# Kernel tuning notes

Hardware: AMD Instinct MI355X
Metric: run time of the kernel (lower is better)

Reference implementation:

```python
import jax, jax.numpy as jnp
from jax import lax
import numpy as np

GROUPS = 32

def setup_inputs() -> dict:
    key = jax.random.key(0)
    ks = jax.random.split(key, 12)
    B, C, H, O, N = 4, 256, 256, 256, 4096
    s = 0.02  # small init scale to keep logits in a stable range
    x  = jax.random.normal(ks[0], (B, C, N), dtype=jnp.float32)
    Wk = jax.random.normal(ks[1], (H, C), dtype=jnp.float32) * s
    bk = jax.random.normal(ks[2], (H,), dtype=jnp.float32) * s
    Wq = jax.random.normal(ks[3], (H, C), dtype=jnp.float32) * s
    bq = jax.random.normal(ks[4], (H,), dtype=jnp.float32) * s
    W1 = jax.random.normal(ks[5], (H, C), dtype=jnp.float32) * s
    b1 = jax.random.normal(ks[6], (H,), dtype=jnp.float32) * s
    # grouped conv1d kernel: (out_ch, in_ch // groups, kw) in 'OIH' layout
    W2 = jax.random.normal(ks[7], (H, H // GROUPS, 3), dtype=jnp.float32) * s
    b2 = jax.random.normal(ks[8], (H,), dtype=jnp.float32) * s
    W3 = jax.random.normal(ks[9], (O, H), dtype=jnp.float32) * s
    b3 = jax.random.normal(ks[10], (O,), dtype=jnp.float32) * s
    return {"x": x, "Wk": Wk, "bk": bk, "Wq": Wq, "bq": bq,
            "W1": W1, "b1": b1, "W2": W2, "b2": b2, "W3": W3, "b3": b3}


def reference(x, Wk, bk, Wq, bq, W1, b1, W2, b2, W3, b3):
    # k: 1x1 conv then permute(0,2,1) -> [B, N, H]
    k = jnp.einsum('hc,bcn->bnh', Wk, x) + bk
    # q: 1x1 conv -> [B, H, N]
    q = jnp.einsum('hc,bcn->bhn', Wq, x) + bq[None, :, None]
    # sim = softmax(k @ q, dim=-2): softmax over the FIRST N axis (rows)
    sim = jax.nn.softmax(jnp.einsum('bnh,bhm->bnm', k, q), axis=-2)  # [B, N, N]
    # v path: 1x1 conv -> grouped 3-tap conv (pad=1) -> ReLU -> 1x1 conv
    v1 = jnp.einsum('hc,bcn->bhn', W1, x) + b1[None, :, None]
    v2 = lax.conv_general_dilated(
        v1, W2, window_strides=(1,), padding='SAME',
        feature_group_count=GROUPS,
        dimension_numbers=('NCH', 'OIH', 'NCH')) + b2[None, :, None]
    v2 = jax.nn.relu(v2)
    v = jnp.einsum('oh,bhn->bon', W3, v2) + b3[None, :, None]  # [B, O, N]
    # out = v @ sim -> [B, O, N]
    return jnp.einsum('bon,bnm->bom', v, sim)
```

## Files before the change

### kernel.cpp

```cpp
#include <hip/hip_runtime.h>


#define B_ 4
#define C_ 256
#define H_ 256
#define O_ 256
#define N_ 4096
#define NSPLIT 4
#define SPAN (N_ / NSPLIT)
#define ITERS (SPAN / 32)

typedef short short8 __attribute__((ext_vector_type(8)));
typedef float floatx4 __attribute__((ext_vector_type(4)));
typedef float floatx16 __attribute__((ext_vector_type(16)));
typedef unsigned uint2v __attribute__((ext_vector_type(2)));

__device__ __forceinline__ unsigned short f2bf(float f) {
  unsigned u = __float_as_uint(f);
  u = (u + 0x7fffu + ((u >> 16) & 1u)) >> 16;
  return (unsigned short)u;
}
__device__ __forceinline__ float bf2f(unsigned short u) {
  return __uint_as_float(((unsigned)u) << 16);
}
__device__ __forceinline__ floatx4 mfma16(short8 a, short8 b, floatx4 c) {
  return __builtin_amdgcn_mfma_f32_16x16x32_bf16(a, b, c, 0, 0, 0);
}
__device__ __forceinline__ floatx16 mfma32(short8 a, short8 b, floatx16 c) {
  return __builtin_amdgcn_mfma_f32_32x32x16_bf16(a, b, c, 0, 0, 0);
}
__device__ __forceinline__ unsigned pack2bf(float a, float b) {
  return __builtin_amdgcn_perm(__float_as_uint(b) + 0x8000u,
                               __float_as_uint(a) + 0x8000u, 0x07060302u);
}

__global__ __launch_bounds__(256) void prep_w_kernel(
    const float* __restrict__ Wk, const float* __restrict__ Wq,
    const float* __restrict__ W1, const float* __restrict__ W3,
    unsigned short* __restrict__ wk, unsigned short* __restrict__ wq,
    unsigned short* __restrict__ w1, unsigned short* __restrict__ w3) {
  const int i = blockIdx.x * 256 + threadIdx.x;
  wk[i] = f2bf(Wk[i]);
  wq[i] = f2bf(Wq[i]);
  w1[i] = f2bf(W1[i]);
  w3[i] = f2bf(W3[i]);
}

__global__ __launch_bounds__(256) void gemm1_kernel(
    const float* __restrict__ x,
    const unsigned short* __restrict__ wk,
    const float* __restrict__ bk, const float* __restrict__ bq,
    const float* __restrict__ b1,
    unsigned short* __restrict__ ko, unsigned short* __restrict__ qo,
    unsigned short* __restrict__ v1o) {
  __shared__ unsigned short xL[32][264];

  const int blk  = blockIdx.x;
  const int b    = blk >> 7;
  const int nc   = blk & 127;
  const int n032 = nc * 32;
  const int t    = threadIdx.x;

  {
    const int c0 = t >> 3;
    const int nq = t & 7;
    const float* xb = x + ((size_t)b * C_) * N_ + n032 + nq * 4;
#pragma unroll
    for (int i = 0; i < 8; ++i) {
      const int c = c0 + i * 32;
      const floatx4 v = *reinterpret_cast<const floatx4*>(xb + (size_t)c * N_);
#pragma unroll
      for (int j = 0; j < 4; ++j) xL[nq * 4 + j][c] = f2bf(v[j]);
    }
  }
  __syncthreads();

  const int ln  = t & 63;
  const int wv  = t >> 6;
  const int m32 = ln & 31;
  const int hl  = ln >> 5;

  int   uoff[6];
  float ubias[6];
  int   uop[6], utt[6];
#pragma unroll
  for (int u = 0; u < 6; ++u) {
    const int gu = wv * 6 + u;
    const int op = gu >> 3;
    const int tt = gu & 7;
    uop[u] = op;
    utt[u] = tt;
    uoff[u] = op * 65536 + (tt * 32 + m32) * 256 + hl * 8;
    const float* bp = (op == 0) ? bk : ((op == 1) ? bq : b1);
    ubias[u] = bp[tt * 32 + m32];
  }

  floatx16 acc[6];
#pragma unroll
  for (int u = 0; u < 6; ++u)
#pragma unroll
    for (int r = 0; r < 16; ++r) acc[u][r] = 0.f;

#pragma unroll
  for (int ks = 0; ks < 16; ++ks) {
    short8 af = *reinterpret_cast<const short8*>(&xL[m32][ks * 16 + hl * 8]);
#pragma unroll
    for (int u = 0; u < 6; ++u) {
      short8 bf = *reinterpret_cast<const short8*>(wk + uoff[u] + ks * 16);
      acc[u] = mfma32(af, bf, acc[u]);
    }
  }

#pragma unroll
  for (int u = 0; u < 6; ++u) {
    const int h = utt[u] * 32 + m32;
    if (uop[u] == 0) {
      unsigned short* kb = ko + ((size_t)(b * 128 + nc)) * 8192;
      const int eh = (h >> 4) * 512 + ((h >> 3) & 1) * 256 + (h & 7);
#pragma unroll
      for (int r = 0; r < 16; ++r) {
        const int nl = (r & 3) + 8 * (r >> 2) + 4 * hl;
        kb[eh + nl * 8] = f2bf(acc[u][r] + ubias[u]);
      }
    } else {
      unsigned short* o = (uop[u] == 1) ? qo : v1o;
#pragma unroll
      for (int r = 0; r < 16; ++r) {
        const int n = n032 + (r & 3) + 8 * (r >> 2) + 4 * hl;
        o[((size_t)(b * N_ + n)) * H_ + h] = f2bf(acc[u][r] + ubias[u]);
      }
    }
  }
}

__global__ __launch_bounds__(256) void convgemm2_kernel(
    const unsigned short* __restrict__ v1, const float* __restrict__ W2,
    const float* __restrict__ b2, const unsigned short* __restrict__ w3,
    const float* __restrict__ b3, unsigned short* __restrict__ vo) {
  __shared__ unsigned short v2L[32][264];

  const int h   = threadIdx.x;
  const int blk = blockIdx.x;
  const int b   = blk >> 7;
  const int nc  = blk & 127;
  const int n0  = nc * 32;
  const int g8  = h & ~7;

  {
    float w[24];
#pragma unroll
    for (int i = 0; i < 24; ++i) w[i] = W2[h * 24 + i];
    const float bias = b2[h];
    const unsigned short* vb = v1 + (size_t)b * (N_ * H_) + g8;

    float fp[8], fc[8], fn[8];
    if (n0 == 0) {
#pragma unroll
      for (int i = 0; i < 8; ++i) fp[i] = 0.f;
    } else {
      short8 u = *reinterpret_cast<const short8*>(vb + (size_t)(n0 - 1) * H_);
#pragma unroll
      for (int i = 0; i < 8; ++i) fp[i] = bf2f((unsigned short)u[i]);
    }
    {
      short8 u = *reinterpret_cast<const short8*>(vb + (size_t)n0 * H_);
#pragma unroll
      for (int i = 0; i < 8; ++i) fc[i] = bf2f((unsigned short)u[i]);
    }
#pragma unroll 1
    for (int ns = 0; ns < 32; ++ns) {
      const int n = n0 + ns;
      if (n + 1 < N_) {
        short8 u = *reinterpret_cast<const short8*>(vb + (size_t)(n + 1) * H_);
#pragma unroll
        for (int i = 0; i < 8; ++i) fn[i] = bf2f((unsigned short)u[i]);
      } else {
#pragma unroll
        for (int i = 0; i < 8; ++i) fn[i] = 0.f;
      }
      float a = bias;
#pragma unroll
      for (int i = 0; i < 8; ++i)
        a += w[i * 3] * fp[i] + w[i * 3 + 1] * fc[i] + w[i * 3 + 2] * fn[i];
      v2L[ns][h] = f2bf(fmaxf(a, 0.f));
#pragma unroll
      for (int i = 0; i < 8; ++i) { fp[i] = fc[i]; fc[i] = fn[i]; }
    }
  }
  __syncthreads();

  const int ln = threadIdx.x & 63;
  const int wv = threadIdx.x >> 6;
  const int m  = ln & 31;
  const int hl = ln >> 5;

  floatx16 acc2[2];
#pragma unroll
  for (int ot = 0; ot < 2; ++ot)
#pragma unroll
    for (int r = 0; r < 16; ++r) acc2[ot][r] = 0.f;

#pragma unroll
  for (int ks = 0; ks < 16; ++ks) {
    short8 bfr = *reinterpret_cast<const short8*>(&v2L[m][ks * 16 + hl * 8]);
#pragma unroll
    for (int ot = 0; ot < 2; ++ot) {
      const int o0 = wv * 64 + ot * 32;
      short8 afr = *reinterpret_cast<const short8*>(
          w3 + (o0 + m) * H_ + ks * 16 + hl * 8);
      acc2[ot] = mfma32(afr, bfr, acc2[ot]);
    }
  }

  const int kn = (m >> 4) & 1;
  const int nl = m & 15;
  unsigned short* vkn = vo + ((size_t)(b * 128 + nc) * 2 + kn) * 4096;
#pragma unroll
  for (int ot = 0; ot < 2; ++ot)
#pragma unroll
    for (int r = 0; r < 16; ++r) {
      const int o = wv * 64 + ot * 32 + (r & 3) + 8 * (r >> 2) + 4 * hl;
      vkn[(o >> 5) * 512 + (nl >> 3) * 256 + (o & 31) * 8 + (nl & 7)] =
          f2bf(acc2[ot][r] + b3[o]);
    }
}

__global__ __launch_bounds__(512, 2) void attn_kernel(
    const unsigned short* __restrict__ kbf, const unsigned short* __restrict__ qbf,
    const unsigned short* __restrict__ vbf,
    unsigned short* __restrict__ pacc, float* __restrict__ pml) {
  __shared__ __attribute__((aligned(16))) char smem[7][16384];

  const int tid = threadIdx.x;
  const int ln  = tid & 63;
  const int wv  = tid >> 6;
  const int gid = blockIdx.x;
  const int b   = gid & 3;
  const int s   = (gid >> 2) & 3;
  const int mt256 = gid >> 4;
  const int mt32  = mt256 * 8 + wv;
  const int m0  = mt32 * 32;
  const int m   = ln & 31;
  const int hl  = ln >> 5;
  const bool grpB = (wv >= 4);
  const int lane_base = ln * 16;

  const unsigned short* qrow = qbf + ((size_t)b * N_ + m0 + m) * H_ + hl * 8;
  short8 qf[16];
#pragma unroll
  for (int ks = 0; ks < 16; ++ks)
    qf[ks] = *reinterpret_cast<const short8*>(qrow + ks * 16);

  floatx16 acc[8];
#pragma unroll
  for (int t = 0; t < 8; ++t)
#pragma unroll
    for (int r = 0; r < 16; ++r) acc[t][r] = 0.f;
  float Lp = 0.f;

  const size_t row0 = (size_t)(b * 128 + s * 32);

  auto stage = [&](int nc) {
    const char* kg = (const char*)(kbf + (row0 + nc) * 8192);
    const char* vg = (const char*)(vbf + (row0 + nc) * 8192);
    char* lk = &smem[nc % 3][0];
    char* lv = &smem[3 + (nc & 3)][0];
#pragma unroll
    for (int j = 0; j < 2; ++j) {
      const int ofs = j * 8192 + tid * 16;
      __builtin_amdgcn_global_load_lds(
          (const __attribute__((address_space(1))) void*)(kg + ofs),
          (__attribute__((address_space(3))) void*)(lk + ofs), 16, 0, 0);
      __builtin_amdgcn_global_load_lds(
          (const __attribute__((address_space(1))) void*)(vg + ofs),
          (__attribute__((address_space(3))) void*)(lv + ofs), 16, 0, 0);
    }
  };

  short8 pf0, pf1;

  auto qk = [&](const char* sk) -> floatx16 {
    floatx16 sacc;
#pragma unroll
    for (int r = 0; r < 16; ++r) sacc[r] = 0.f;
    __builtin_amdgcn_s_setprio(1);
#pragma unroll
    for (int ks = 0; ks < 16; ++ks) {
      short8 kf = *reinterpret_cast<const short8*>(sk + lane_base + ks * 1024);
      sacc = mfma32(kf, qf[ks], sacc);
    }
    __builtin_amdgcn_s_setprio(0);
    return sacc;
  };
  auto pv = [&](const char* sv) {
    __builtin_amdgcn_s_setprio(1);
#pragma unroll
    for (int ot = 0; ot < 8; ++ot) {
      short8 vf0 = *reinterpret_cast<const short8*>(sv + lane_base + ot * 1024);
      short8 vf1 = *reinterpret_cast<const short8*>(
          sv + lane_base + 8192 + ot * 1024);
      acc[ot] = mfma32(vf0, pf0, acc[ot]);
      acc[ot] = mfma32(vf1, pf1, acc[ot]);
    }
    __builtin_amdgcn_s_setprio(0);
  };
  auto softmax = [&](floatx16 sacc) {
#if __has_builtin(__builtin_amdgcn_permlane32_swap)
    unsigned d[8];
#pragma unroll
    for (int i = 0; i < 8; ++i) {
      const float a = __expf(sacc[2 * i]);
      const float bb = __expf(sacc[2 * i + 1]);
      Lp += a + bb;
      d[i] = pack2bf(a, bb);
    }
#pragma unroll
    for (int g = 0; g < 2; ++g) {
      uint2v r0 = __builtin_amdgcn_permlane32_swap(d[4 * g + 0], d[4 * g + 2],
                                                   false, false);
      uint2v r1 = __builtin_amdgcn_permlane32_swap(d[4 * g + 1], d[4 * g + 3],
                                                   false, false);
      d[4 * g + 0] = r0.x; d[4 * g + 2] = r0.y;
      d[4 * g + 1] = r1.x; d[4 * g + 3] = r1.y;
    }
    union { unsigned u[4]; short8 s8; } c0, c1;
    c0.u[0] = d[0]; c0.u[1] = d[1]; c0.u[2] = d[2]; c0.u[3] = d[3];
    c1.u[0] = d[4]; c1.u[1] = d[5]; c1.u[2] = d[6]; c1.u[3] = d[7];
    pf0 = c0.s8;
    pf1 = c1.s8;
#else
    float pv_[16];
#pragma unroll
    for (int r = 0; r < 16; ++r) { pv_[r] = __expf(sacc[r]); Lp += pv_[r]; }
    unsigned wpk[8];
#pragma unroll
    for (int r4 = 0; r4 < 4; ++r4) {
      wpk[r4]     = pack2bf(pv_[r4], pv_[r4 + 4]);
      wpk[r4 + 4] = pack2bf(pv_[r4 + 8], pv_[r4 + 12]);
    }
    const int hlsh = hl * 16;
#pragma unroll
    for (int j = 0; j < 8; ++j) {
      const int srcLane = m + ((j >> 2) << 5);
      const int u0 = __shfl((int)wpk[j & 3],       srcLane);
      const int u1 = __shfl((int)wpk[(j & 3) + 4], srcLane);
      pf0[j] = (short)((unsigned)u0 >> hlsh);
      pf1[j] = (short)((unsigned)u1 >> hlsh);
    }
#endif
  };

  stage(0);
  stage(1);

#pragma unroll 1
  for (int nc = 0; nc < ITERS; ++nc) {
    if (nc + 1 < ITERS) {
      asm volatile("s_waitcnt vmcnt(4)\n\ts_barrier" ::: "memory");
    } else {
      asm volatile("s_waitcnt vmcnt(0)\n\ts_barrier" ::: "memory");
    }
    __builtin_amdgcn_sched_barrier(0);
    if (nc + 2 < ITERS) stage(nc + 2);

    const char* sk = &smem[nc % 3][0];

    if (!grpB) {
      floatx16 sacc = qk(sk);
      softmax(sacc);
      pv(&smem[3 + (nc & 3)][0]);
    } else {
      if (nc > 0) pv(&smem[3 + ((nc - 1) & 3)][0]);
      floatx16 sacc = qk(sk);
      softmax(sacc);
    }
  }
  if (grpB) pv(&smem[3 + ((ITERS - 1) & 3)][0]);

  float Lv = Lp + __shfl_xor(Lp, 32);
  const float invL = 1.f / Lv;

  const int pwid = (b * 128 + mt32) * NSPLIT + s;
  unsigned short* pa = pacc + (size_t)pwid * (O_ * 32);
#pragma unroll
  for (int ot = 0; ot < 8; ++ot)
#pragma unroll
    for (int r = 0; r < 16; ++r) {
      const int o = ot * 32 + (r & 3) + 8 * (r >> 2) + 4 * hl;
      pa[o * 32 + m] = f2bf(acc[ot][r] * invL);
    }
  if (hl == 0) pml[pwid * 32 + m] = Lv;
}

__global__ __launch_bounds__(256) void combine_kernel(
    const unsigned short* __restrict__ pacc, const float* __restrict__ pml,
    float* __restrict__ out) {
  const int blk = blockIdx.x;
  const int b   = blk >> 7;
  const int mw  = blk & 127;
  const int o   = threadIdx.x;
  const int base = (b * 128 + mw) * NSPLIT;

  __shared__ float w[NSPLIT][32];
  if (threadIdx.x < 32) {
    const int c = threadIdx.x;
    float L[NSPLIT], sum = 0.f;
#pragma unroll
    for (int sp = 0; sp < NSPLIT; ++sp) {
      L[sp] = pml[(base + sp) * 32 + c];
      sum += L[sp];
    }
    const float inv = 1.f / sum;
#pragma unroll
    for (int sp = 0; sp < NSPLIT; ++sp) w[sp][c] = L[sp] * inv;
  }
  __syncthreads();

  float res[32];
#pragma unroll
  for (int c = 0; c < 32; ++c) res[c] = 0.f;
#pragma unroll
  for (int sp = 0; sp < NSPLIT; ++sp) {
    const unsigned short* pa =
        pacc + (size_t)(base + sp) * (O_ * 32) + o * 32;
#pragma unroll
    for (int c8 = 0; c8 < 4; ++c8) {
      short8 u = *reinterpret_cast<const short8*>(pa + c8 * 8);
#pragma unroll
      for (int i = 0; i < 8; ++i)
        res[c8 * 8 + i] =
            fmaf(w[sp][c8 * 8 + i], bf2f((unsigned short)u[i]), res[c8 * 8 + i]);
    }
  }
  float* ob = out + ((size_t)(b * O_ + o)) * N_ + mw * 32;
#pragma unroll
  for (int c4 = 0; c4 < 8; ++c4) {
    floatx4 v4 = {res[c4 * 4], res[c4 * 4 + 1], res[c4 * 4 + 2], res[c4 * 4 + 3]};
    *reinterpret_cast<floatx4*>(ob + c4 * 4) = v4;
  }
}

extern "C" void kernel_launch(void* const* d_in, const int* in_sizes, int n_in,
                              void* d_out, int out_size, void* d_ws, size_t ws_size,
                              hipStream_t stream) {
  const float* x  = (const float*)d_in[0];
  const float* Wk = (const float*)d_in[1];
  const float* bk = (const float*)d_in[2];
  const float* Wq = (const float*)d_in[3];
  const float* bq = (const float*)d_in[4];
  const float* W1 = (const float*)d_in[5];
  const float* b1 = (const float*)d_in[6];
  const float* W2 = (const float*)d_in[7];
  const float* b2 = (const float*)d_in[8];
  const float* W3 = (const float*)d_in[9];
  const float* b3 = (const float*)d_in[10];
  float* out = (float*)d_out;

  char* ws = (char*)d_ws;
  const size_t SZ = (size_t)B_ * N_ * H_ * sizeof(unsigned short);
  unsigned short* wkbf = (unsigned short*)(ws);
  unsigned short* wqbf = (unsigned short*)(ws + 131072);
  unsigned short* w1bf = (unsigned short*)(ws + 262144);
  unsigned short* w3bf = (unsigned short*)(ws + 393216);
  char* base = ws + 524288;
  unsigned short* kbf  = (unsigned short*)(base);
  unsigned short* qbf  = (unsigned short*)(base + SZ);
  unsigned short* vbf  = (unsigned short*)(base + 2 * SZ);
  unsigned short* v1bf = (unsigned short*)(base + 3 * SZ);
  unsigned short* pacc = (unsigned short*)(base + 3 * SZ);
  float*          pml  = (float*)(base + 7 * SZ);

  prep_w_kernel<<<256, 256, 0, stream>>>(
      Wk, Wq, W1, W3, wkbf, wqbf, w1bf, w3bf);
  gemm1_kernel<<<512, 256, 0, stream>>>(x, wkbf, bk, bq, b1,
                                        kbf, qbf, v1bf);
  convgemm2_kernel<<<512, 256, 0, stream>>>(v1bf, W2, b2, w3bf, b3, vbf);
  attn_kernel<<<256, 512, 0, stream>>>(kbf, qbf, vbf, pacc, pml);
  combine_kernel<<<512, 256, 0, stream>>>(pacc, pml, out);
}
```

Measured before the change: 221.2 us.

## Fuse projection GEMM, grouped conv and W3 GEMM into one kernel with halo

```diff
diff --git a/kernel.cpp b/kernel.cpp
--- a/kernel.cpp
+++ b/kernel.cpp
@@ -22,9 +22,6 @@
 }
 __device__ __forceinline__ float bf2f(unsigned short u) {
   return __uint_as_float(((unsigned)u) << 16);
-}
-__device__ __forceinline__ floatx4 mfma16(short8 a, short8 b, floatx4 c) {
-  return __builtin_amdgcn_mfma_f32_16x16x32_bf16(a, b, c, 0, 0, 0);
 }
 __device__ __forceinline__ floatx16 mfma32(short8 a, short8 b, floatx16 c) {
   return __builtin_amdgcn_mfma_f32_32x32x16_bf16(a, b, c, 0, 0, 0);
@@ -46,14 +43,18 @@
   w3[i] = f2bf(W3[i]);
 }
 
-__global__ __launch_bounds__(256) void gemm1_kernel(
+__global__ __launch_bounds__(256) void fused1_kernel(
     const float* __restrict__ x,
     const unsigned short* __restrict__ wk,
     const float* __restrict__ bk, const float* __restrict__ bq,
     const float* __restrict__ b1,
+    const float* __restrict__ W2, const float* __restrict__ b2,
+    const unsigned short* __restrict__ w3, const float* __restrict__ b3,
     unsigned short* __restrict__ ko, unsigned short* __restrict__ qo,
-    unsigned short* __restrict__ v1o) {
-  __shared__ unsigned short xL[32][264];
+    unsigned short* __restrict__ vo) {
+  __shared__ unsigned short xL[34][264];
+  __shared__ unsigned short v1L[34][264];
+  __shared__ unsigned short v2L[32][264];
 
   const int blk  = blockIdx.x;
   const int b    = blk >> 7;
@@ -70,8 +71,17 @@
       const int c = c0 + i * 32;
       const floatx4 v = *reinterpret_cast<const floatx4*>(xb + (size_t)c * N_);
 #pragma unroll
-      for (int j = 0; j < 4; ++j) xL[nq * 4 + j][c] = f2bf(v[j]);
-    }
+      for (int j = 0; j < 4; ++j) xL[1 + nq * 4 + j][c] = f2bf(v[j]);
+    }
+  }
+  {
+    const int c = t;
+    const float lv =
+        (n032 == 0) ? 0.f : x[((size_t)(b * C_ + c)) * N_ + n032 - 1];
+    const float rv =
+        (n032 + 32 >= N_) ? 0.f : x[((size_t)(b * C_ + c)) * N_ + n032 + 32];
+    xL[0][c] = f2bf(lv);
+    xL[33][c] = f2bf(rv);
   }
   __syncthreads();
 
@@ -80,104 +90,100 @@
   const int m32 = ln & 31;
   const int hl  = ln >> 5;
 
-  int   uoff[6];
-  float ubias[6];
-  int   uop[6], utt[6];
-#pragma unroll
-  for (int u = 0; u < 6; ++u) {
-    const int gu = wv * 6 + u;
-    const int op = gu >> 3;
-    const int tt = gu & 7;
-    uop[u] = op;
-    utt[u] = tt;
-    uoff[u] = op * 65536 + (tt * 32 + m32) * 256 + hl * 8;
+  {
+    const int op    = (wv <= 1) ? wv : 2;
+    const int abase = (wv <= 1) ? 1 : ((wv == 2) ? 0 : 2);
     const float* bp = (op == 0) ? bk : ((op == 1) ? bq : b1);
-    ubias[u] = bp[tt * 32 + m32];
-  }
-
-  floatx16 acc[6];
-#pragma unroll
-  for (int u = 0; u < 6; ++u)
-#pragma unroll
-    for (int r = 0; r < 16; ++r) acc[u][r] = 0.f;
-
-#pragma unroll
-  for (int ks = 0; ks < 16; ++ks) {
-    short8 af = *reinterpret_cast<const short8*>(&xL[m32][ks * 16 + hl * 8]);
-#pragma unroll
-    for (int u = 0; u < 6; ++u) {
-      short8 bf = *reinterpret_cast<const short8*>(wk + uoff[u] + ks * 16);
-      acc[u] = mfma32(af, bf, acc[u]);
-    }
-  }
-
-#pragma unroll
-  for (int u = 0; u < 6; ++u) {
-    const int h = utt[u] * 32 + m32;
-    if (uop[u] == 0) {
+
+    float ubias[8];
+    int   uoff[8];
+#pragma unroll
+    for (int u = 0; u < 8; ++u) {
+      uoff[u]  = op * 65536 + (u * 32 + m32) * 256 + hl * 8;
+      ubias[u] = bp[u * 32 + m32];
+    }
+
+    floatx16 acc[8];
+#pragma unroll
+    for (int u = 0; u < 8; ++u)
+#pragma unroll
+      for (int r = 0; r < 16; ++r) acc[u][r] = 0.f;
+
+#pragma unroll
+    for (int ks = 0; ks < 16; ++ks) {
+      short8 af =
+          *reinterpret_cast<const short8*>(&xL[abase + m32][ks * 16 + hl * 8]);
+#pragma unroll
+      for (int u = 0; u < 8; ++u) {
+        short8 bf = *reinterpret_cast<const short8*>(wk + uoff[u] + ks * 16);
+        acc[u] = mfma32(af, bf, acc[u]);
+      }
+    }
+
+    if (wv == 0) {
       unsigned short* kb = ko + ((size_t)(b * 128 + nc)) * 8192;
-      const int eh = (h >> 4) * 512 + ((h >> 3) & 1) * 256 + (h & 7);
-#pragma unroll
-      for (int r = 0; r < 16; ++r) {
-        const int nl = (r & 3) + 8 * (r >> 2) + 4 * hl;
-        kb[eh + nl * 8] = f2bf(acc[u][r] + ubias[u]);
+#pragma unroll
+      for (int u = 0; u < 8; ++u) {
+        const int h = u * 32 + m32;
+        const int eh = (h >> 4) * 512 + ((h >> 3) & 1) * 256 + (h & 7);
+#pragma unroll
+        for (int r = 0; r < 16; ++r) {
+          const int nl = (r & 3) + 8 * (r >> 2) + 4 * hl;
+          kb[eh + nl * 8] = f2bf(acc[u][r] + ubias[u]);
+        }
+      }
+    } else if (wv == 1) {
+#pragma unroll
+      for (int u = 0; u < 8; ++u) {
+        const int h = u * 32 + m32;
+#pragma unroll
+        for (int r = 0; r < 16; ++r) {
+          const int n = n032 + (r & 3) + 8 * (r >> 2) + 4 * hl;
+          qo[((size_t)(b * N_ + n)) * H_ + h] = f2bf(acc[u][r] + ubias[u]);
+        }
       }
     } else {
-      unsigned short* o = (uop[u] == 1) ? qo : v1o;
-#pragma unroll
-      for (int r = 0; r < 16; ++r) {
-        const int n = n032 + (r & 3) + 8 * (r >> 2) + 4 * hl;
-        o[((size_t)(b * N_ + n)) * H_ + h] = f2bf(acc[u][r] + ubias[u]);
-      }
-    }
-  }
-}
-
-__global__ __launch_bounds__(256) void convgemm2_kernel(
-    const unsigned short* __restrict__ v1, const float* __restrict__ W2,
-    const float* __restrict__ b2, const unsigned short* __restrict__ w3,
-    const float* __restrict__ b3, unsigned short* __restrict__ vo) {
-  __shared__ unsigned short v2L[32][264];
-
-  const int h   = threadIdx.x;
-  const int blk = blockIdx.x;
-  const int b   = blk >> 7;
-  const int nc  = blk & 127;
-  const int n0  = nc * 32;
-  const int g8  = h & ~7;
+      const int cofs = (wv == 2) ? 0 : 2;
+#pragma unroll
+      for (int u = 0; u < 8; ++u) {
+        const int h = u * 32 + m32;
+#pragma unroll
+        for (int r = 0; r < 16; ++r) {
+          const int col = cofs + (r & 3) + 8 * (r >> 2) + 4 * hl;
+          v1L[col][h] = f2bf(acc[u][r] + ubias[u]);
+        }
+      }
+    }
+  }
+  __syncthreads();
+
+  if (n032 == 0) v1L[0][t] = 0;
+  if (n032 + 32 >= N_) v1L[33][t] = 0;
+  __syncthreads();
 
   {
+    const int h  = t;
+    const int g8 = h & ~7;
     float w[24];
 #pragma unroll
     for (int i = 0; i < 24; ++i) w[i] = W2[h * 24 + i];
     const float bias = b2[h];
-    const unsigned short* vb = v1 + (size_t)b * (N_ * H_) + g8;
 
     float fp[8], fc[8], fn[8];
-    if (n0 == 0) {
-#pragma unroll
-      for (int i = 0; i < 8; ++i) fp[i] = 0.f;
-    } else {
-      short8 u = *reinterpret_cast<const short8*>(vb + (size_t)(n0 - 1) * H_);
-#pragma unroll
-      for (int i = 0; i < 8; ++i) fp[i] = bf2f((unsigned short)u[i]);
-    }
     {
-      short8 u = *reinterpret_cast<const short8*>(vb + (size_t)n0 * H_);
-#pragma unroll
-      for (int i = 0; i < 8; ++i) fc[i] = bf2f((unsigned short)u[i]);
+      short8 u0 = *reinterpret_cast<const short8*>(&v1L[0][g8]);
+      short8 u1 = *reinterpret_cast<const short8*>(&v1L[1][g8]);
+#pragma unroll
+      for (int i = 0; i < 8; ++i) {
+        fp[i] = bf2f((unsigned short)u0[i]);
+        fc[i] = bf2f((unsigned short)u1[i]);
+      }
     }
 #pragma unroll 1
     for (int ns = 0; ns < 32; ++ns) {
-      const int n = n0 + ns;
-      if (n + 1 < N_) {
-        short8 u = *reinterpret_cast<const short8*>(vb + (size_t)(n + 1) * H_);
-#pragma unroll
-        for (int i = 0; i < 8; ++i) fn[i] = bf2f((unsigned short)u[i]);
-      } else {
-#pragma unroll
-        for (int i = 0; i < 8; ++i) fn[i] = 0.f;
-      }
+      short8 un = *reinterpret_cast<const short8*>(&v1L[ns + 2][g8]);
+#pragma unroll
+      for (int i = 0; i < 8; ++i) fn[i] = bf2f((unsigned short)un[i]);
       float a = bias;
 #pragma unroll
       for (int i = 0; i < 8; ++i)
@@ -189,40 +195,38 @@
   }
   __syncthreads();
 
-  const int ln = threadIdx.x & 63;
-  const int wv = threadIdx.x >> 6;
-  const int m  = ln & 31;
-  const int hl = ln >> 5;
-
-  floatx16 acc2[2];
-#pragma unroll
-  for (int ot = 0; ot < 2; ++ot)
-#pragma unroll
-    for (int r = 0; r < 16; ++r) acc2[ot][r] = 0.f;
-
-#pragma unroll
-  for (int ks = 0; ks < 16; ++ks) {
-    short8 bfr = *reinterpret_cast<const short8*>(&v2L[m][ks * 16 + hl * 8]);
-#pragma unroll
-    for (int ot = 0; ot < 2; ++ot) {
-      const int o0 = wv * 64 + ot * 32;
-      short8 afr = *reinterpret_cast<const short8*>(
-          w3 + (o0 + m) * H_ + ks * 16 + hl * 8);
-      acc2[ot] = mfma32(afr, bfr, acc2[ot]);
-    }
-  }
-
-  const int kn = (m >> 4) & 1;
-  const int nl = m & 15;
-  unsigned short* vkn = vo + ((size_t)(b * 128 + nc) * 2 + kn) * 4096;
-#pragma unroll
-  for (int ot = 0; ot < 2; ++ot)
-#pragma unroll
-    for (int r = 0; r < 16; ++r) {
-      const int o = wv * 64 + ot * 32 + (r & 3) + 8 * (r >> 2) + 4 * hl;
-      vkn[(o >> 5) * 512 + (nl >> 3) * 256 + (o & 31) * 8 + (nl & 7)] =
-          f2bf(acc2[ot][r] + b3[o]);
-    }
+  {
+    const int m  = m32;
+    floatx16 acc2[2];
+#pragma unroll
+    for (int ot = 0; ot < 2; ++ot)
+#pragma unroll
+      for (int r = 0; r < 16; ++r) acc2[ot][r] = 0.f;
+
+#pragma unroll
+    for (int ks = 0; ks < 16; ++ks) {
+      short8 bfr = *reinterpret_cast<const short8*>(&v2L[m][ks * 16 + hl * 8]);
+#pragma unroll
+      for (int ot = 0; ot < 2; ++ot) {
+        const int o0 = wv * 64 + ot * 32;
+        short8 afr = *reinterpret_cast<const short8*>(
+            w3 + (o0 + m) * H_ + ks * 16 + hl * 8);
+        acc2[ot] = mfma32(afr, bfr, acc2[ot]);
+      }
+    }
+
+    const int kn = (m >> 4) & 1;
+    const int nl = m & 15;
+    unsigned short* vkn = vo + ((size_t)(b * 128 + nc) * 2 + kn) * 4096;
+#pragma unroll
+    for (int ot = 0; ot < 2; ++ot)
+#pragma unroll
+      for (int r = 0; r < 16; ++r) {
+        const int o = wv * 64 + ot * 32 + (r & 3) + 8 * (r >> 2) + 4 * hl;
+        vkn[(o >> 5) * 512 + (nl >> 3) * 256 + (o & 31) * 8 + (nl & 7)] =
+            f2bf(acc2[ot][r] + b3[o]);
+      }
+  }
 }
 
 __global__ __launch_bounds__(512, 2) void attn_kernel(
@@ -466,15 +470,13 @@
   unsigned short* kbf  = (unsigned short*)(base);
   unsigned short* qbf  = (unsigned short*)(base + SZ);
   unsigned short* vbf  = (unsigned short*)(base + 2 * SZ);
-  unsigned short* v1bf = (unsigned short*)(base + 3 * SZ);
   unsigned short* pacc = (unsigned short*)(base + 3 * SZ);
   float*          pml  = (float*)(base + 7 * SZ);
 
   prep_w_kernel<<<256, 256, 0, stream>>>(
       Wk, Wq, W1, W3, wkbf, wqbf, w1bf, w3bf);
-  gemm1_kernel<<<512, 256, 0, stream>>>(x, wkbf, bk, bq, b1,
-                                        kbf, qbf, v1bf);
-  convgemm2_kernel<<<512, 256, 0, stream>>>(v1bf, W2, b2, w3bf, b3, vbf);
+  fused1_kernel<<<512, 256, 0, stream>>>(x, wkbf, bk, bq, b1, W2, b2,
+                                         w3bf, b3, kbf, qbf, vbf);
   attn_kernel<<<256, 512, 0, stream>>>(kbf, qbf, vbf, pacc, pml);
   combine_kernel<<<512, 256, 0, stream>>>(pacc, pml, out);
 }
```

After: 230.4 us. 1.04x slower.
